# Kernel optimization log

Hardware: AMD Instinct MI355X
Metric: run time of the kernel (lower is better)

## Reference

```python
import jax, jax.numpy as jnp
import numpy as np

B, S, D, H = 2, 2048, 1024, 16
DK = D // H


def setup_inputs() -> dict:
    key = jax.random.key(0)
    ks = jax.random.split(key, 8)
    std = 0.02
    inp = {
        "query": jax.random.normal(ks[0], (B, S, D), jnp.float32),
        "key": jax.random.normal(ks[1], (B, S, D), jnp.float32),
        "value": jax.random.normal(ks[2], (B, S, D), jnp.float32),
        # causal mask, 1 = attend, 0 = masked (matches masked_fill(mask==0, -1e9))
        "mask": jnp.broadcast_to(
            jnp.tril(jnp.ones((S, S), jnp.int32))[None, None], (B, 1, S, S)
        ),
        "wq_w": jax.random.normal(ks[3], (D, D), jnp.float32) * std,
        "wq_b": jnp.zeros((D,), jnp.float32),
        "wk_w": jax.random.normal(ks[4], (D, D), jnp.float32) * std,
        "wk_b": jnp.zeros((D,), jnp.float32),
        "wv_w": jax.random.normal(ks[5], (D, D), jnp.float32) * std,
        "wv_b": jnp.zeros((D,), jnp.float32),
        "wo_w": jax.random.normal(ks[6], (D, D), jnp.float32) * std,
        "wo_b": jnp.zeros((D,), jnp.float32),
    }
    return inp


def _split_heads(x, b):
    # [B, S, D] -> [B, H, S, DK]
    return x.reshape(b, -1, H, DK).transpose(0, 2, 1, 3)


def reference(query, key, value, mask, wq_w, wq_b, wk_w, wk_b, wv_w, wv_b, wo_w, wo_b):
    b = query.shape[0]
    q = _split_heads(query @ wq_w.T + wq_b, b)
    k = _split_heads(key @ wk_w.T + wk_b, b)
    v = _split_heads(value @ wv_w.T + wv_b, b)

    scale = 1.0 / np.sqrt(DK).astype(np.float32)
    scores = jnp.einsum("bhqd,bhkd->bhqk", q, k) * scale  # [B,H,Sq,Sk]
    scores = jnp.where(mask == 0, jnp.float32(-1e9), scores)
    attn = jax.nn.softmax(scores, axis=-1)  # dropout p=0 (eval)

    ctx = jnp.einsum("bhqk,bhkd->bhqd", attn, v)  # [B,H,Sq,DK]
    ctx = ctx.transpose(0, 2, 1, 3).reshape(b, -1, D)  # [B,Sq,D]
    out = ctx @ wo_w.T + wo_b
    return out, attn
```

## Files before the change

### kernel.cpp

```cpp
#include <hip/hip_runtime.h>

#define B_ 2
#define S_ 2048
#define D_ 1024
#define H_ 16
#define DK_ 64

typedef __attribute__((ext_vector_type(8))) short bf16x8;
typedef __attribute__((ext_vector_type(4))) float f32x4;

#define MFMA16(a, b, c) __builtin_amdgcn_mfma_f32_16x16x32_bf16((a), (b), (c), 0, 0, 0)

__device__ __forceinline__ unsigned short f2bf(float f) {
  union { float f; unsigned u; } x; x.f = f;
  return (unsigned short)((x.u + 0x7fffu + ((x.u >> 16) & 1u)) >> 16);
}

__device__ __forceinline__ void gload_lds16(const void* g, void* l) {
  __builtin_amdgcn_global_load_lds((const __attribute__((address_space(1))) void*)g,
                                   (__attribute__((address_space(3))) void*)l, 16, 0, 0);
}

__global__ __launch_bounds__(256) void cvt_all(
    const float* __restrict__ s0, const float* __restrict__ s1, const float* __restrict__ s2,
    const float* __restrict__ s3, const float* __restrict__ s4, const float* __restrict__ s5,
    const float* __restrict__ s6,
    unsigned short* __restrict__ d0, unsigned short* __restrict__ d1,
    unsigned short* __restrict__ d2, unsigned short* __restrict__ d3,
    unsigned short* __restrict__ d4, unsigned short* __restrict__ d5,
    unsigned short* __restrict__ d6, int nbig, int nsmall) {
  const float* src; unsigned short* dst; int n4;
  switch (blockIdx.y) {
    case 0: src = s0; dst = d0; n4 = nbig; break;
    case 1: src = s1; dst = d1; n4 = nbig; break;
    case 2: src = s2; dst = d2; n4 = nbig; break;
    case 3: src = s3; dst = d3; n4 = nsmall; break;
    case 4: src = s4; dst = d4; n4 = nsmall; break;
    case 5: src = s5; dst = d5; n4 = nsmall; break;
    default: src = s6; dst = d6; n4 = nsmall; break;
  }
  int i = blockIdx.x * blockDim.x + threadIdx.x;
  int stride = gridDim.x * blockDim.x;
  for (; i < n4; i += stride) {
    float4 v = ((const float4*)src)[i];
    ushort4 o;
    o.x = f2bf(v.x); o.y = f2bf(v.y); o.z = f2bf(v.z); o.w = f2bf(v.w);
    ((ushort4*)dst)[i] = o;
  }
}

__device__ __forceinline__ void gemm_body(const unsigned short* __restrict__ A,
                                          const unsigned short* __restrict__ W,
                                          const float* __restrict__ bias,
                                          void* __restrict__ out,
                                          int mode, float scale, int tm, int tn) {
  __shared__ __align__(16) unsigned short lsA[128 * 32];
  __shared__ __align__(16) unsigned short lsB[128 * 32];
  const int K = 1024;
  const int tid = threadIdx.x;
  const int w = tid >> 6, l = tid & 63;
  const int wm = w >> 2, wn = w & 3;
  const int cl = l & 15, lg = l >> 4;

  f32x4 acc[4][2];
#pragma unroll
  for (int i = 0; i < 4; ++i)
#pragma unroll
    for (int j = 0; j < 2; ++j) acc[i][j] = (f32x4){0.f, 0.f, 0.f, 0.f};

  const int srow = w * 16 + (l >> 2);
  const int slog = (l & 3) ^ ((srow >> 1) & 3);
  const unsigned short* Abase = A + (size_t)(tm * 128 + srow) * K + slog * 8;
  const unsigned short* Wbase = W + (size_t)(tn * 128 + srow) * K + slog * 8;
  unsigned short* ldA = lsA + w * 512;
  unsigned short* ldB = lsB + w * 512;

  for (int ks = 0; ks < 32; ++ks) {
    const int k0 = ks * 32;
    gload_lds16(Abase + k0, ldA);
    gload_lds16(Wbase + k0, ldB);
    __syncthreads();

    bf16x8 af[4], bfr[2];
#pragma unroll
    for (int f = 0; f < 4; ++f) {
      int ar = wm * 64 + f * 16 + cl;
      int ph = lg ^ ((ar >> 1) & 3);
      af[f] = *(const bf16x8*)(lsA + ar * 32 + ph * 8);
    }
#pragma unroll
    for (int f = 0; f < 2; ++f) {
      int br = wn * 32 + f * 16 + cl;
      int ph = lg ^ ((br >> 1) & 3);
      bfr[f] = *(const bf16x8*)(lsB + br * 32 + ph * 8);
    }
#pragma unroll
    for (int i = 0; i < 4; ++i)
#pragma unroll
      for (int j = 0; j < 2; ++j) acc[i][j] = MFMA16(af[i], bfr[j], acc[i][j]);
    __syncthreads();
  }

#pragma unroll
  for (int i = 0; i < 4; ++i) {
#pragma unroll
    for (int j = 0; j < 2; ++j) {
#pragma unroll
      for (int r = 0; r < 4; ++r) {
        int mm = tm * 128 + wm * 64 + i * 16 + 4 * lg + r;
        int nn = tn * 128 + wn * 32 + j * 16 + cl;
        float v = (acc[i][j][r] + bias[nn]) * scale;
        if (mode == 2) {
          ((float*)out)[(size_t)mm * 1024 + nn] = v;
        } else {
          int bb = mm >> 11, s = mm & 2047, hh = nn >> 6, dk = nn & 63;
          size_t idx = (mode == 0)
                           ? ((((size_t)bb * H_ + hh) * S_ + s) * DK_ + dk)
                           : ((((size_t)bb * H_ + hh) * DK_ + dk) * S_ + s);
          ((unsigned short*)out)[idx] = f2bf(v);
        }
      }
    }
  }
}

#define QSCALE 0.18033688011112042f

__global__ __launch_bounds__(512) void gemm_qkv(
    const unsigned short* __restrict__ xq, const unsigned short* __restrict__ xk,
    const unsigned short* __restrict__ xv, const unsigned short* __restrict__ wq,
    const unsigned short* __restrict__ wk, const unsigned short* __restrict__ wv,
    const float* __restrict__ bq, const float* __restrict__ bk, const float* __restrict__ bv,
    unsigned short* __restrict__ oq, unsigned short* __restrict__ ok,
    unsigned short* __restrict__ ov) {
  const int z = blockIdx.z;
  const unsigned short* A = (z == 0) ? xq : (z == 1) ? xk : xv;
  const unsigned short* W = (z == 0) ? wq : (z == 1) ? wk : wv;
  const float* bias = (z == 0) ? bq : (z == 1) ? bk : bv;
  void* out = (z == 0) ? (void*)oq : (z == 1) ? (void*)ok : (void*)ov;
  gemm_body(A, W, bias, out, (z == 2) ? 1 : 0, (z == 0) ? QSCALE : 1.0f,
            blockIdx.x, blockIdx.y);
}

__global__ __launch_bounds__(512) void gemm_out(const unsigned short* __restrict__ A,
                                                const unsigned short* __restrict__ W,
                                                const float* __restrict__ bias,
                                                float* __restrict__ out) {
  gemm_body(A, W, bias, out, 2, 1.0f, blockIdx.x, blockIdx.y);
}

__global__ __launch_bounds__(256) void attn_fused(const unsigned short* __restrict__ qh,
                                                  const unsigned short* __restrict__ kh,
                                                  const unsigned short* __restrict__ vt,
                                                  float* __restrict__ attn,
                                                  unsigned short* __restrict__ ctxh) {
  __shared__ __align__(16) unsigned short kst[2][4096];
  __shared__ __align__(16) unsigned short vst[2][4096];
  __shared__ __align__(16) unsigned short pbuf[4][16 * 72];
  const int wgid = blockIdx.x;
  const int y = wgid >> 3;
  const int qt = 31 - (y >> 2);
  const int bh = (wgid & 7) * 4 + (y & 3);
  const int b = bh >> 4, h = bh & 15;
  const int w = threadIdx.x >> 6, l = threadIdx.x & 63;
  const int cl = l & 15, lg = l >> 4;
  const int qrb = qt * 64 + w * 16;
  const int qloc = w * 16 + cl;

  const unsigned short* kbh = kh + (size_t)bh * S_ * DK_;
  const unsigned short* vbh = vt + (size_t)bh * DK_ * S_;

  bf16x8 aq0, aq1;
  {
    const unsigned short* qp = qh + (size_t)bh * S_ * DK_ + (size_t)(qrb + cl) * DK_ + lg * 8;
    aq0 = *(const bf16x8*)qp;
    aq1 = *(const bf16x8*)(qp + 32);
  }

  const int sr0 = w * 16 + (l >> 3);
  const int sc = l & 7;
  auto stageK = [&](int kt, int buf) {
    const char* base = (const char*)kbh + (size_t)kt * 8192;
#pragma unroll
    for (int call = 0; call < 2; ++call) {
      int r = sr0 + call * 8;
      gload_lds16(base + r * 128 + ((sc ^ (r & 7)) << 4),
                  (char*)kst[buf] + w * 2048 + call * 1024);
    }
  };
  auto stageV = [&](int kt, int buf) {
    const char* base = (const char*)vbh + (size_t)kt * 128;
#pragma unroll
    for (int call = 0; call < 2; ++call) {
      int r = sr0 + call * 8;
      gload_lds16(base + (size_t)r * (S_ * 2) + ((sc ^ (r & 7)) << 4),
                  (char*)vst[buf] + w * 2048 + call * 1024);
    }
  };
  auto readK = [&](int buf, bf16x8(&k0)[4], bf16x8(&k1)[4]) {
#pragma unroll
    for (int mt = 0; mt < 4; ++mt) {
      int r = mt * 16 + cl;
      const char* rb = (const char*)kst[buf] + r * 128;
      k0[mt] = *(const bf16x8*)(rb + ((lg ^ (r & 7)) << 4));
      k1[mt] = *(const bf16x8*)(rb + (((4 + lg) ^ (r & 7)) << 4));
    }
  };

  f32x4 lsv = (f32x4){0.f, 0.f, 0.f, 0.f};
  stageK(0, 0);
  __syncthreads();
  for (int t = 0; t <= qt; ++t) {
    const int cur = t & 1;
    if (t < qt) stageK(t + 1, cur ^ 1);
    bf16x8 k0[4], k1[4];
    readK(cur, k0, k1);
    f32x4 cc[4];
#pragma unroll
    for (int mt = 0; mt < 4; ++mt) {
      f32x4 c = (f32x4){0.f, 0.f, 0.f, 0.f};
      c = MFMA16(k0[mt], aq0, c);
      cc[mt] = MFMA16(k1[mt], aq1, c);
    }
    const bool diag = (t == qt);
#pragma unroll
    for (int mt = 0; mt < 4; ++mt)
#pragma unroll
      for (int r = 0; r < 4; ++r) {
        float e = exp2f(cc[mt][r]);
        if (diag && (mt * 16 + 4 * lg + r > qloc)) e = 0.f;
        lsv[r] += e;
      }
    __syncthreads();
  }
  float ls = (lsv[0] + lsv[1]) + (lsv[2] + lsv[3]);
  ls += __shfl_xor(ls, 16);
  ls += __shfl_xor(ls, 32);
  const float inv = 1.0f / ls;

  f32x4 pv[4];
#pragma unroll
  for (int i = 0; i < 4; ++i) pv[i] = (f32x4){0.f, 0.f, 0.f, 0.f};
  unsigned short* pw = pbuf[w];
  float* arow = attn + (size_t)bh * S_ * S_ + (size_t)(qrb + cl) * S_;

  stageK(0, 0);
  stageV(0, 0);
  __syncthreads();
  for (int t = 0; t <= qt; ++t) {
    const int cur = t & 1;
    if (t < qt) {
      stageK(t + 1, cur ^ 1);
      stageV(t + 1, cur ^ 1);
    }
    bf16x8 k0[4], k1[4];
    readK(cur, k0, k1);
    f32x4 cc[4];
#pragma unroll
    for (int mt = 0; mt < 4; ++mt) {
      f32x4 c = (f32x4){0.f, 0.f, 0.f, 0.f};
      c = MFMA16(k0[mt], aq0, c);
      cc[mt] = MFMA16(k1[mt], aq1, c);
    }
    const bool diag = (t == qt);
#pragma unroll
    for (int mt = 0; mt < 4; ++mt) {
      f32x4 pf;
      ushort4 pb;
#pragma unroll
      for (int r = 0; r < 4; ++r) {
        float p = exp2f(cc[mt][r]) * inv;
        if (diag && (mt * 16 + 4 * lg + r > qloc)) p = 0.f;
        pf[r] = p;
        ((unsigned short*)&pb)[r] = f2bf(p);
      }
      *(f32x4*)(arow + t * 64 + mt * 16 + 4 * lg) = pf;
      *(ushort4*)(pw + cl * 72 + mt * 16 + 4 * lg) = pb;
    }
#pragma unroll
    for (int c2 = 0; c2 < 2; ++c2) {
      bf16x8 pa = *(const bf16x8*)(pw + cl * 72 + c2 * 32 + 8 * lg);
#pragma unroll
      for (int n2 = 0; n2 < 4; ++n2) {
        int r = n2 * 16 + cl;
        const char* rb = (const char*)vst[cur] + r * 128;
        bf16x8 vb = *(const bf16x8*)(rb + (((c2 * 4 + lg) ^ (r & 7)) << 4));
        pv[n2] = MFMA16(pa, vb, pv[n2]);
      }
    }
    __syncthreads();
  }

  {
    float* zrow = attn + (size_t)bh * S_ * S_ + (size_t)(qrb + (l >> 2)) * S_;
    const f32x4 z = (f32x4){0.f, 0.f, 0.f, 0.f};
    for (int c = (qt + 1) * 64 + (l & 3) * 16; c < S_; c += 64) {
      *(f32x4*)(zrow + c) = z;
      *(f32x4*)(zrow + c + 4) = z;
      *(f32x4*)(zrow + c + 8) = z;
      *(f32x4*)(zrow + c + 12) = z;
    }
  }

#pragma unroll
  for (int n2 = 0; n2 < 4; ++n2)
#pragma unroll
    for (int r = 0; r < 4; ++r)
      ctxh[((size_t)b * S_ + qrb + 4 * lg + r) * D_ + h * DK_ + n2 * 16 + cl] =
          f2bf(pv[n2][r]);
}

extern "C" void kernel_launch(void* const* d_in, const int* in_sizes, int n_in,
                              void* d_out, int out_size, void* d_ws, size_t ws_size,
                              hipStream_t stream) {
  const float* q  = (const float*)d_in[0];
  const float* k  = (const float*)d_in[1];
  const float* v  = (const float*)d_in[2];
  const float* wq = (const float*)d_in[4];
  const float* bq = (const float*)d_in[5];
  const float* wk = (const float*)d_in[6];
  const float* bk = (const float*)d_in[7];
  const float* wv = (const float*)d_in[8];
  const float* bv = (const float*)d_in[9];
  const float* wo = (const float*)d_in[10];
  const float* bo = (const float*)d_in[11];

  float* out  = (float*)d_out;
  float* attn = out + (size_t)B_ * S_ * D_;

  char* ws = (char*)d_ws;
  const size_t MB = 1024 * 1024;
  unsigned short* xq   = (unsigned short*)(ws + 0 * MB);
  unsigned short* xk   = (unsigned short*)(ws + 8 * MB);
  unsigned short* xv   = (unsigned short*)(ws + 16 * MB);
  unsigned short* wqb  = (unsigned short*)(ws + 24 * MB);
  unsigned short* wkb  = (unsigned short*)(ws + 26 * MB);
  unsigned short* wvb  = (unsigned short*)(ws + 28 * MB);
  unsigned short* wob  = (unsigned short*)(ws + 30 * MB);
  unsigned short* qhb  = (unsigned short*)(ws + 32 * MB);
  unsigned short* khb  = (unsigned short*)(ws + 40 * MB);
  unsigned short* vtb  = (unsigned short*)(ws + 48 * MB);
  unsigned short* ctxh = (unsigned short*)(ws + 56 * MB);

  const int NX4 = (B_ * S_ * D_) / 4;
  const int NW4 = (D_ * D_) / 4;
  cvt_all<<<dim3(256, 7), 256, 0, stream>>>(q, k, v, wq, wk, wv, wo,
                                            xq, xk, xv, wqb, wkb, wvb, wob, NX4, NW4);

  gemm_qkv<<<dim3(32, 8, 3), 512, 0, stream>>>(xq, xk, xv, wqb, wkb, wvb,
                                               bq, bk, bv, qhb, khb, vtb);

  attn_fused<<<dim3(1024), 256, 0, stream>>>(qhb, khb, vtb, attn, ctxh);

  gemm_out<<<dim3(32, 8), 512, 0, stream>>>(ctxh, wob, bo, out);
}
```

Baseline: 291.6 us.

## Fuse fp32-to-bf16 conversion into GEMM loads and tune attention barriers

Removes the separate conversion kernel. The GEMMs now load fp32 activations and weights directly, convert them to bf16 in registers and store them to LDS, saving a launch and a round trip through workspace. It also raises wave priority around MFMA blocks and replaces attention loop barriers with a partial vmcnt wait plus a raw s_barrier to keep prefetches in flight. The trade-off is that the GEMM now reads twice the bytes per tile and loses the async direct-to-LDS load path, and the partial wait count relies on an assumed number of outstanding loads.

```diff
diff --git a/kernel.cpp b/kernel.cpp
--- a/kernel.cpp
+++ b/kernel.cpp
@@ -1,4 +1,5 @@
 #include <hip/hip_runtime.h>
+#include <hip/hip_bf16.h>
 
 #define B_ 2
 #define S_ 2048
@@ -16,41 +17,22 @@
   return (unsigned short)((x.u + 0x7fffu + ((x.u >> 16) & 1u)) >> 16);
 }
 
+__device__ __forceinline__ bf16x8 pack8(float4 a, float4 b) {
+  bf16x8 r;
+  r[0] = (short)f2bf(a.x); r[1] = (short)f2bf(a.y);
+  r[2] = (short)f2bf(a.z); r[3] = (short)f2bf(a.w);
+  r[4] = (short)f2bf(b.x); r[5] = (short)f2bf(b.y);
+  r[6] = (short)f2bf(b.z); r[7] = (short)f2bf(b.w);
+  return r;
+}
+
 __device__ __forceinline__ void gload_lds16(const void* g, void* l) {
   __builtin_amdgcn_global_load_lds((const __attribute__((address_space(1))) void*)g,
                                    (__attribute__((address_space(3))) void*)l, 16, 0, 0);
 }
 
-__global__ __launch_bounds__(256) void cvt_all(
-    const float* __restrict__ s0, const float* __restrict__ s1, const float* __restrict__ s2,
-    const float* __restrict__ s3, const float* __restrict__ s4, const float* __restrict__ s5,
-    const float* __restrict__ s6,
-    unsigned short* __restrict__ d0, unsigned short* __restrict__ d1,
-    unsigned short* __restrict__ d2, unsigned short* __restrict__ d3,
-    unsigned short* __restrict__ d4, unsigned short* __restrict__ d5,
-    unsigned short* __restrict__ d6, int nbig, int nsmall) {
-  const float* src; unsigned short* dst; int n4;
-  switch (blockIdx.y) {
-    case 0: src = s0; dst = d0; n4 = nbig; break;
-    case 1: src = s1; dst = d1; n4 = nbig; break;
-    case 2: src = s2; dst = d2; n4 = nbig; break;
-    case 3: src = s3; dst = d3; n4 = nsmall; break;
-    case 4: src = s4; dst = d4; n4 = nsmall; break;
-    case 5: src = s5; dst = d5; n4 = nsmall; break;
-    default: src = s6; dst = d6; n4 = nsmall; break;
-  }
-  int i = blockIdx.x * blockDim.x + threadIdx.x;
-  int stride = gridDim.x * blockDim.x;
-  for (; i < n4; i += stride) {
-    float4 v = ((const float4*)src)[i];
-    ushort4 o;
-    o.x = f2bf(v.x); o.y = f2bf(v.y); o.z = f2bf(v.z); o.w = f2bf(v.w);
-    ((ushort4*)dst)[i] = o;
-  }
-}
-
-__device__ __forceinline__ void gemm_body(const unsigned short* __restrict__ A,
-                                          const unsigned short* __restrict__ W,
+template <bool A_BF16>
+__device__ __forceinline__ void gemm_body(const void* Ap, const float* __restrict__ Wf,
                                           const float* __restrict__ bias,
                                           void* __restrict__ out,
                                           int mode, float scale, int tm, int tn) {
@@ -68,17 +50,30 @@
 #pragma unroll
     for (int j = 0; j < 2; ++j) acc[i][j] = (f32x4){0.f, 0.f, 0.f, 0.f};
 
-  const int srow = w * 16 + (l >> 2);
-  const int slog = (l & 3) ^ ((srow >> 1) & 3);
-  const unsigned short* Abase = A + (size_t)(tm * 128 + srow) * K + slog * 8;
-  const unsigned short* Wbase = W + (size_t)(tn * 128 + srow) * K + slog * 8;
-  unsigned short* ldA = lsA + w * 512;
-  unsigned short* ldB = lsB + w * 512;
+  const int sr = w * 16 + (l >> 2);
+  const int sg = l & 3;
+  const int gsl = sg ^ ((sr >> 1) & 3);
+  const unsigned short* Ab16 = (const unsigned short*)Ap + (size_t)(tm * 128 + sr) * K + gsl * 8;
+  const float* Af32 = (const float*)Ap + (size_t)(tm * 128 + sr) * K + gsl * 8;
+  const float* Wb = Wf + (size_t)(tn * 128 + sr) * K + gsl * 8;
+  unsigned short* ldsA_gl = lsA + w * 512;
+  unsigned short* dwA = lsA + sr * 32 + sg * 8;
+  unsigned short* dwB = lsB + sr * 32 + sg * 8;
 
   for (int ks = 0; ks < 32; ++ks) {
     const int k0 = ks * 32;
-    gload_lds16(Abase + k0, ldA);
-    gload_lds16(Wbase + k0, ldB);
+    if constexpr (A_BF16) {
+      gload_lds16(Ab16 + k0, ldsA_gl);
+    } else {
+      float4 a0 = *(const float4*)(Af32 + k0);
+      float4 a1 = *(const float4*)(Af32 + k0 + 4);
+      *(bf16x8*)dwA = pack8(a0, a1);
+    }
+    {
+      float4 b0 = *(const float4*)(Wb + k0);
+      float4 b1 = *(const float4*)(Wb + k0 + 4);
+      *(bf16x8*)dwB = pack8(b0, b1);
+    }
     __syncthreads();
 
     bf16x8 af[4], bfr[2];
@@ -94,10 +89,12 @@
       int ph = lg ^ ((br >> 1) & 3);
       bfr[f] = *(const bf16x8*)(lsB + br * 32 + ph * 8);
     }
+    __builtin_amdgcn_s_setprio(1);
 #pragma unroll
     for (int i = 0; i < 4; ++i)
 #pragma unroll
       for (int j = 0; j < 2; ++j) acc[i][j] = MFMA16(af[i], bfr[j], acc[i][j]);
+    __builtin_amdgcn_s_setprio(0);
     __syncthreads();
   }
 
@@ -127,26 +124,25 @@
 #define QSCALE 0.18033688011112042f
 
 __global__ __launch_bounds__(512) void gemm_qkv(
-    const unsigned short* __restrict__ xq, const unsigned short* __restrict__ xk,
-    const unsigned short* __restrict__ xv, const unsigned short* __restrict__ wq,
-    const unsigned short* __restrict__ wk, const unsigned short* __restrict__ wv,
+    const float* __restrict__ xq, const float* __restrict__ xk, const float* __restrict__ xv,
+    const float* __restrict__ wq, const float* __restrict__ wk, const float* __restrict__ wv,
     const float* __restrict__ bq, const float* __restrict__ bk, const float* __restrict__ bv,
     unsigned short* __restrict__ oq, unsigned short* __restrict__ ok,
     unsigned short* __restrict__ ov) {
   const int z = blockIdx.z;
-  const unsigned short* A = (z == 0) ? xq : (z == 1) ? xk : xv;
-  const unsigned short* W = (z == 0) ? wq : (z == 1) ? wk : wv;
+  const float* A = (z == 0) ? xq : (z == 1) ? xk : xv;
+  const float* W = (z == 0) ? wq : (z == 1) ? wk : wv;
   const float* bias = (z == 0) ? bq : (z == 1) ? bk : bv;
   void* out = (z == 0) ? (void*)oq : (z == 1) ? (void*)ok : (void*)ov;
-  gemm_body(A, W, bias, out, (z == 2) ? 1 : 0, (z == 0) ? QSCALE : 1.0f,
-            blockIdx.x, blockIdx.y);
+  gemm_body<false>(A, W, bias, out, (z == 2) ? 1 : 0, (z == 0) ? QSCALE : 1.0f,
+                   blockIdx.x, blockIdx.y);
 }
 
 __global__ __launch_bounds__(512) void gemm_out(const unsigned short* __restrict__ A,
-                                                const unsigned short* __restrict__ W,
+                                                const float* __restrict__ W,
                                                 const float* __restrict__ bias,
                                                 float* __restrict__ out) {
-  gemm_body(A, W, bias, out, 2, 1.0f, blockIdx.x, blockIdx.y);
+  gemm_body<true>(A, W, bias, out, 2, 1.0f, blockIdx.x, blockIdx.y);
 }
 
 __global__ __launch_bounds__(256) void attn_fused(const unsigned short* __restrict__ qh,
@@ -216,12 +212,14 @@
     bf16x8 k0[4], k1[4];
     readK(cur, k0, k1);
     f32x4 cc[4];
+    __builtin_amdgcn_s_setprio(1);
 #pragma unroll
     for (int mt = 0; mt < 4; ++mt) {
       f32x4 c = (f32x4){0.f, 0.f, 0.f, 0.f};
       c = MFMA16(k0[mt], aq0, c);
       cc[mt] = MFMA16(k1[mt], aq1, c);
     }
+    __builtin_amdgcn_s_setprio(0);
     const bool diag = (t == qt);
 #pragma unroll
     for (int mt = 0; mt < 4; ++mt)
@@ -246,7 +244,8 @@
 
   stageK(0, 0);
   stageV(0, 0);
-  __syncthreads();
+  asm volatile("s_waitcnt vmcnt(0)" ::: "memory");
+  __builtin_amdgcn_s_barrier();
   for (int t = 0; t <= qt; ++t) {
     const int cur = t & 1;
     if (t < qt) {
@@ -256,12 +255,14 @@
     bf16x8 k0[4], k1[4];
     readK(cur, k0, k1);
     f32x4 cc[4];
+    __builtin_amdgcn_s_setprio(1);
 #pragma unroll
     for (int mt = 0; mt < 4; ++mt) {
       f32x4 c = (f32x4){0.f, 0.f, 0.f, 0.f};
       c = MFMA16(k0[mt], aq0, c);
       cc[mt] = MFMA16(k1[mt], aq1, c);
     }
+    __builtin_amdgcn_s_setprio(0);
     const bool diag = (t == qt);
 #pragma unroll
     for (int mt = 0; mt < 4; ++mt) {
@@ -277,6 +278,7 @@
       *(f32x4*)(arow + t * 64 + mt * 16 + 4 * lg) = pf;
       *(ushort4*)(pw + cl * 72 + mt * 16 + 4 * lg) = pb;
     }
+    __builtin_amdgcn_s_setprio(1);
 #pragma unroll
     for (int c2 = 0; c2 < 2; ++c2) {
       bf16x8 pa = *(const bf16x8*)(pw + cl * 72 + c2 * 32 + 8 * lg);
@@ -288,7 +290,9 @@
         pv[n2] = MFMA16(pa, vb, pv[n2]);
       }
     }
-    __syncthreads();
+    __builtin_amdgcn_s_setprio(0);
+    asm volatile("s_waitcnt vmcnt(4)" ::: "memory");
+    __builtin_amdgcn_s_barrier();
   }
 
   {
@@ -330,27 +334,15 @@
 
   char* ws = (char*)d_ws;
   const size_t MB = 1024 * 1024;
-  unsigned short* xq   = (unsigned short*)(ws + 0 * MB);
-  unsigned short* xk   = (unsigned short*)(ws + 8 * MB);
-  unsigned short* xv   = (unsigned short*)(ws + 16 * MB);
-  unsigned short* wqb  = (unsigned short*)(ws + 24 * MB);
-  unsigned short* wkb  = (unsigned short*)(ws + 26 * MB);
-  unsigned short* wvb  = (unsigned short*)(ws + 28 * MB);
-  unsigned short* wob  = (unsigned short*)(ws + 30 * MB);
-  unsigned short* qhb  = (unsigned short*)(ws + 32 * MB);
-  unsigned short* khb  = (unsigned short*)(ws + 40 * MB);
-  unsigned short* vtb  = (unsigned short*)(ws + 48 * MB);
-  unsigned short* ctxh = (unsigned short*)(ws + 56 * MB);
-
-  const int NX4 = (B_ * S_ * D_) / 4;
-  const int NW4 = (D_ * D_) / 4;
-  cvt_all<<<dim3(256, 7), 256, 0, stream>>>(q, k, v, wq, wk, wv, wo,
-                                            xq, xk, xv, wqb, wkb, wvb, wob, NX4, NW4);
-
-  gemm_qkv<<<dim3(32, 8, 3), 512, 0, stream>>>(xq, xk, xv, wqb, wkb, wvb,
+  unsigned short* qhb  = (unsigned short*)(ws + 0 * MB);
+  unsigned short* khb  = (unsigned short*)(ws + 8 * MB);
+  unsigned short* vtb  = (unsigned short*)(ws + 16 * MB);
+  unsigned short* ctxh = (unsigned short*)(ws + 24 * MB);
+
+  gemm_qkv<<<dim3(32, 8, 3), 512, 0, stream>>>(q, k, v, wq, wk, wv,
                                                bq, bk, bv, qhb, khb, vtb);
 
   attn_fused<<<dim3(1024), 256, 0, stream>>>(qhb, khb, vtb, attn, ctxh);
 
-  gemm_out<<<dim3(32, 8), 512, 0, stream>>>(ctxh, wob, bo, out);
-}
+  gemm_out<<<dim3(32, 8), 512, 0, stream>>>(ctxh, wo, bo, out);
+}
```

Result: slower. 308.0 us (+5.6%).
